# Optimization experiments

Hardware: AMD Instinct MI355X
Metric: run time of the kernel (lower is better)

## Reference

```python
import jax, jax.numpy as jnp
import numpy as np
import math

L = 16
DECAY = math.exp(-1.0 / 10.0)   # exp(-dt/tau)
THRESHOLD = 1.0
ALPHA = 0.01
EPS = 1e-6


def spike_fn(x):
    # MultiBitSurrogate forward: floor then clamp to [0, L]
    return jnp.clip(jnp.floor(x), 0.0, float(L))


def setup_inputs() -> dict:
    key = jax.random.key(0)
    k1, k2 = jax.random.split(key)
    B, S, D, H = 8, 4096, 512, 512
    x = jax.random.normal(k1, (B, S, D), dtype=jnp.float32)
    W = jax.random.normal(k2, (H, D), dtype=jnp.float32) * (1.0 / math.sqrt(D))
    b = jnp.zeros((H,), dtype=jnp.float32)
    return {"x": x, "W": W, "b": b}


def reference(x, W, b):
    B, S, D = x.shape
    H = W.shape[0]
    # dense input current for all timesteps: (B, S, H)
    h = jnp.einsum('bsd,hd->bsh', x, W) + b

    v0 = jnp.zeros((B, H), dtype=x.dtype)
    theta0 = jnp.full((B, H), THRESHOLD, dtype=x.dtype)

    def step(carry, i_t):
        v, theta = carry
        v = v * DECAY + i_t
        clamp_limit = L * theta * 2.0
        v = jnp.clip(v, -clamp_limit, clamp_limit)
        normalized_v = v / (theta + EPS)
        spike = spike_fn(normalized_v)
        v = v - spike * theta
        theta = theta + ALPHA * spike - ALPHA * (theta - THRESHOLD)
        return (v, theta), spike

    h_t = jnp.swapaxes(h, 0, 1)  # (S, B, H) for scan over time
    (v, theta), spikes = jax.lax.scan(step, (v0, theta0), h_t)
    spikes = jnp.swapaxes(spikes, 0, 1)  # (B, S, H)
    return spikes, v, theta
```

## Files before the change

kernel.cpp:

```cpp
#include <hip/hip_runtime.h>

#define B_DIM 8
#define S_LEN 4096
#define D_DIM 512
#define H_DIM 512

#define DECAY_F 0.90483743f
#define ALPHA_F 0.01f
#define EPS_F   1e-6f

#define KT 16
__global__ __launch_bounds__(256) void gemm_kernel(const float* __restrict__ x,
                                                   const float* __restrict__ W,
                                                   const float* __restrict__ bias,
                                                   float* __restrict__ out) {
    __shared__ float As[KT][132];
    __shared__ float Bs[KT][132];

    const int tid = threadIdx.x;
    const int waveId = tid >> 6;
    const int waveR = waveId & 1;
    const int waveC = waveId >> 1;
    const int lane = tid & 63;
    const int tr = lane >> 3;
    const int tc = lane & 7;
    const int rbase = waveR * 64 + tr * 8;
    const int c0 = waveC * 64 + tc * 4;
    const int c1 = c0 + 32;
    const int bm = blockIdx.y * 128;
    const int bn = blockIdx.x * 128;

    const int lrow = tid >> 2;
    const int lk4  = (tid & 3) * 4;

    const float* xa = &x[(size_t)(bm + lrow) * D_DIM + lk4];
    const float* xb = &x[(size_t)(bm + lrow + 64) * D_DIM + lk4];
    const float* wa = &W[(size_t)(bn + lrow) * D_DIM + lk4];
    const float* wb = &W[(size_t)(bn + lrow + 64) * D_DIM + lk4];

    float acc[8][8];
#pragma unroll
    for (int i = 0; i < 8; ++i)
#pragma unroll
        for (int j = 0; j < 8; ++j) acc[i][j] = 0.f;

    float4 a0 = *reinterpret_cast<const float4*>(xa);
    float4 a1 = *reinterpret_cast<const float4*>(xb);
    float4 b0 = *reinterpret_cast<const float4*>(wa);
    float4 b1 = *reinterpret_cast<const float4*>(wb);

    for (int kk = 0; kk < D_DIM; kk += KT) {
        __syncthreads();
        As[lk4 + 0][lrow]      = a0.x;
        As[lk4 + 1][lrow]      = a0.y;
        As[lk4 + 2][lrow]      = a0.z;
        As[lk4 + 3][lrow]      = a0.w;
        As[lk4 + 0][lrow + 64] = a1.x;
        As[lk4 + 1][lrow + 64] = a1.y;
        As[lk4 + 2][lrow + 64] = a1.z;
        As[lk4 + 3][lrow + 64] = a1.w;
        Bs[lk4 + 0][lrow]      = b0.x;
        Bs[lk4 + 1][lrow]      = b0.y;
        Bs[lk4 + 2][lrow]      = b0.z;
        Bs[lk4 + 3][lrow]      = b0.w;
        Bs[lk4 + 0][lrow + 64] = b1.x;
        Bs[lk4 + 1][lrow + 64] = b1.y;
        Bs[lk4 + 2][lrow + 64] = b1.z;
        Bs[lk4 + 3][lrow + 64] = b1.w;
        __syncthreads();

        if (kk + KT < D_DIM) {
            a0 = *reinterpret_cast<const float4*>(xa + kk + KT);
            a1 = *reinterpret_cast<const float4*>(xb + kk + KT);
            b0 = *reinterpret_cast<const float4*>(wa + kk + KT);
            b1 = *reinterpret_cast<const float4*>(wb + kk + KT);
        }

#pragma unroll
        for (int k = 0; k < KT; ++k) {
            const float4 av0 = *reinterpret_cast<const float4*>(&As[k][rbase]);
            const float4 av1 = *reinterpret_cast<const float4*>(&As[k][rbase + 4]);
            const float4 bv0 = *reinterpret_cast<const float4*>(&Bs[k][c0]);
            const float4 bv1 = *reinterpret_cast<const float4*>(&Bs[k][c1]);
            const float am[8]  = {av0.x, av0.y, av0.z, av0.w, av1.x, av1.y, av1.z, av1.w};
            const float bn_[8] = {bv0.x, bv0.y, bv0.z, bv0.w, bv1.x, bv1.y, bv1.z, bv1.w};
#pragma unroll
            for (int i = 0; i < 8; ++i)
#pragma unroll
                for (int j = 0; j < 8; ++j) acc[i][j] += am[i] * bn_[j];
        }
    }

    const float4 bias0 = *reinterpret_cast<const float4*>(&bias[bn + c0]);
    const float4 bias1 = *reinterpret_cast<const float4*>(&bias[bn + c1]);
    const float bb[8] = {bias0.x, bias0.y, bias0.z, bias0.w, bias1.x, bias1.y, bias1.z, bias1.w};

#pragma unroll
    for (int i = 0; i < 8; ++i) {
        const size_t row = (size_t)(bm + rbase + i);
        float4 o0, o1;
        o0.x = acc[i][0] + bb[0]; o0.y = acc[i][1] + bb[1];
        o0.z = acc[i][2] + bb[2]; o0.w = acc[i][3] + bb[3];
        o1.x = acc[i][4] + bb[4]; o1.y = acc[i][5] + bb[5];
        o1.z = acc[i][6] + bb[6]; o1.w = acc[i][7] + bb[7];
        *reinterpret_cast<float4*>(&out[row * H_DIM + bn + c0]) = o0;
        *reinterpret_cast<float4*>(&out[row * H_DIM + bn + c1]) = o1;
    }
}


__device__ __forceinline__ void stage_chunk(const float* __restrict__ gio, float* dstbase,
                                            int c, int lane) {
    const float* src = gio + (size_t)(c * 32 + (lane >> 4)) * H_DIM + ((lane & 15) << 2);
#pragma unroll
    for (int i = 0; i < 8; ++i) {
        __builtin_amdgcn_global_load_lds(
            (const __attribute__((address_space(1))) void*)(src + (size_t)i * 4 * H_DIM),
            (__attribute__((address_space(3))) void*)(dstbase + i * 256),
            16, 0, 0);
    }
}

__global__ __launch_bounds__(64, 1) void scan_kernel(float* __restrict__ io,
                                                     float* __restrict__ vout,
                                                     float* __restrict__ thout) {
    __shared__ float sbuf[2][32][64];

    const int lane = threadIdx.x;
    const int bi = blockIdx.x;
    const int b = bi >> 3;
    const int h0 = (bi & 7) << 6;

    float* gio = io + (size_t)b * S_LEN * H_DIM + h0;

    float v = 0.f;
    float theta = 1.f;
    float tden = theta + EPS_F;
    float rs = __builtin_amdgcn_rcpf(tden);
    float es = fmaf(-tden, rs, 1.0f);
    float r1 = fmaf(es, rs, rs);
    float es2 = fmaf(-tden, r1, 1.0f);
    float r0 = fmaf(es2, r1, r1);
    float cl = 32.f * theta;
    const float kSixteen = 16.0f;

    stage_chunk(gio, &sbuf[0][0][0], 0, lane);
    asm volatile("s_waitcnt vmcnt(0)" ::: "memory");

    const int NCHUNK = S_LEN / 32;
    for (int c = 0; c < NCHUNK; ++c) {
        if (c + 1 < NCHUNK) {
            stage_chunk(gio, &sbuf[(c + 1) & 1][0][0], c + 1, lane);
            asm volatile("s_waitcnt vmcnt(40)" ::: "memory");
        } else {
            asm volatile("s_waitcnt vmcnt(32)" ::: "memory");
        }
        __builtin_amdgcn_sched_barrier(0);

        const float* sb = &sbuf[c & 1][0][lane];
        float rr[32];
#pragma unroll
        for (int i = 0; i < 32; ++i) rr[i] = sb[i * 64];
        __builtin_amdgcn_sched_barrier(0);

        float* gout = gio + (size_t)c * 32 * H_DIM + lane;

#pragma unroll
        for (int u = 0; u < 32; ++u) {
            float vv = v * DECAY_F + rr[u];
            asm("v_med3_f32 %0, %0, -%1, %1" : "+v"(vv) : "v"(cl));
            v = vv;

            const float q0 = v * r0;
            const float e1 = fmaf(-tden, q0, v);
            const float nv = fmaf(e1, r0, q0);

            float spike = floorf(nv);
            asm("v_med3_f32 %0, %0, 0, %1" : "+v"(spike) : "v"(kSixteen));

            v = v - spike * theta;
            theta = theta + ALPHA_F * spike - ALPHA_F * (theta - 1.0f);

            tden = theta + EPS_F;
            const float rrcp = __builtin_amdgcn_rcpf(tden);
            const float ee = fmaf(-tden, rrcp, 1.0f);
            const float ra = fmaf(ee, rrcp, rrcp);
            const float ee2 = fmaf(-tden, ra, 1.0f);
            r0 = fmaf(ee2, ra, ra);
            cl = 32.f * theta;

            gout[(size_t)u * H_DIM] = spike;
        }
        __builtin_amdgcn_sched_barrier(0);
    }

    const int chain = b * H_DIM + h0 + lane;
    vout[chain]  = v;
    thout[chain] = theta;
}

extern "C" void kernel_launch(void* const* d_in, const int* in_sizes, int n_in,
                              void* d_out, int out_size, void* d_ws, size_t ws_size,
                              hipStream_t stream) {
    const float* x    = (const float*)d_in[0];
    const float* W    = (const float*)d_in[1];
    const float* bias = (const float*)d_in[2];

    float* out   = (float*)d_out;
    float* vout  = out + (size_t)B_DIM * S_LEN * H_DIM;
    float* thout = vout + B_DIM * H_DIM;

    dim3 grid(H_DIM / 128, (B_DIM * S_LEN) / 128);
    gemm_kernel<<<grid, 256, 0, stream>>>(x, W, bias, out);

    scan_kernel<<<64, 64, 0, stream>>>(out, vout, thout);
}
```

Before: 389.5 us.

## Fuse GEMM and scan into one persistent kernel with per-tile readiness flags

Merges the GEMM and the sequential scan into a single launch. Sixteen scan blocks, four waves each, spin on per-(batch, time-stripe) atomic flags and begin scanning as soon as GEMM blocks publish each 128-row stripe. This overlaps the latency-bound scan with GEMM work instead of running them back to back. The cost is a memset of the flags, spin-waiting blocks that hold CUs, and reliance on the scan blocks being scheduled early; it falls back to two launches when the workspace is too small.

```diff
diff --git a/kernel.cpp b/kernel.cpp
--- a/kernel.cpp
+++ b/kernel.cpp
@@ -10,13 +10,28 @@
 #define EPS_F   1e-6f
 
 #define KT 16
-__global__ __launch_bounds__(256) void gemm_kernel(const float* __restrict__ x,
-                                                   const float* __restrict__ W,
-                                                   const float* __restrict__ bias,
-                                                   float* __restrict__ out) {
-    __shared__ float As[KT][132];
-    __shared__ float Bs[KT][132];
-
+#define NCHUNK (S_LEN / 32)
+#define NSCAN_BLOCKS 16
+
+
+__device__ __forceinline__ void stage_chunk(const float* __restrict__ gio, float* dstbase,
+                                            int c, int lane) {
+    const float* src = gio + (size_t)(c * 32 + (lane >> 4)) * H_DIM + ((lane & 15) << 2);
+#pragma unroll
+    for (int i = 0; i < 8; ++i) {
+        __builtin_amdgcn_global_load_lds(
+            (const __attribute__((address_space(1))) void*)(src + (size_t)i * 4 * H_DIM),
+            (__attribute__((address_space(3))) void*)(dstbase + i * 256),
+            16, 0, 0);
+    }
+}
+
+__device__ __forceinline__ void gemm_tile(const float* __restrict__ x,
+                                          const float* __restrict__ W,
+                                          const float* __restrict__ bias,
+                                          float* __restrict__ out,
+                                          float (*As)[132], float (*Bs)[132],
+                                          int bm, int bn) {
     const int tid = threadIdx.x;
     const int waveId = tid >> 6;
     const int waveR = waveId & 1;
@@ -27,8 +42,6 @@
     const int rbase = waveR * 64 + tr * 8;
     const int c0 = waveC * 64 + tc * 4;
     const int c1 = c0 + 32;
-    const int bm = blockIdx.y * 128;
-    const int bn = blockIdx.x * 128;
 
     const int lrow = tid >> 2;
     const int lk4  = (tid & 3) * 4;
@@ -108,31 +121,10 @@
     }
 }
 
-
-__device__ __forceinline__ void stage_chunk(const float* __restrict__ gio, float* dstbase,
-                                            int c, int lane) {
-    const float* src = gio + (size_t)(c * 32 + (lane >> 4)) * H_DIM + ((lane & 15) << 2);
-#pragma unroll
-    for (int i = 0; i < 8; ++i) {
-        __builtin_amdgcn_global_load_lds(
-            (const __attribute__((address_space(1))) void*)(src + (size_t)i * 4 * H_DIM),
-            (__attribute__((address_space(3))) void*)(dstbase + i * 256),
-            16, 0, 0);
-    }
-}
-
-__global__ __launch_bounds__(64, 1) void scan_kernel(float* __restrict__ io,
-                                                     float* __restrict__ vout,
-                                                     float* __restrict__ thout) {
-    __shared__ float sbuf[2][32][64];
-
-    const int lane = threadIdx.x;
-    const int bi = blockIdx.x;
-    const int b = bi >> 3;
-    const int h0 = (bi & 7) << 6;
-
-    float* gio = io + (size_t)b * S_LEN * H_DIM + h0;
-
+__device__ __forceinline__ void scan_wave(float* __restrict__ gio, float* sbuf,
+                                          const int* flagrow, int lane,
+                                          float* __restrict__ vout,
+                                          float* __restrict__ thout, int chain) {
     float v = 0.f;
     float theta = 1.f;
     float tden = theta + EPS_F;
@@ -144,20 +136,32 @@
     float cl = 32.f * theta;
     const float kSixteen = 16.0f;
 
-    stage_chunk(gio, &sbuf[0][0][0], 0, lane);
+    if (flagrow) {
+        while (__hip_atomic_load(&flagrow[0], __ATOMIC_ACQUIRE, __HIP_MEMORY_SCOPE_AGENT) < 4)
+            __builtin_amdgcn_s_sleep(1);
+    }
+    stage_chunk(gio, sbuf, 0, lane);
     asm volatile("s_waitcnt vmcnt(0)" ::: "memory");
 
-    const int NCHUNK = S_LEN / 32;
     for (int c = 0; c < NCHUNK; ++c) {
         if (c + 1 < NCHUNK) {
-            stage_chunk(gio, &sbuf[(c + 1) & 1][0][0], c + 1, lane);
-            asm volatile("s_waitcnt vmcnt(40)" ::: "memory");
+            if (((c + 1) & 3) == 0 && flagrow) {
+                const int stn = (c + 1) >> 2;
+                while (__hip_atomic_load(&flagrow[stn], __ATOMIC_ACQUIRE,
+                                         __HIP_MEMORY_SCOPE_AGENT) < 4)
+                    __builtin_amdgcn_s_sleep(1);
+                asm volatile("s_waitcnt vmcnt(0)" ::: "memory");
+                stage_chunk(gio, sbuf + ((c + 1) & 1) * 2048, c + 1, lane);
+            } else {
+                stage_chunk(gio, sbuf + ((c + 1) & 1) * 2048, c + 1, lane);
+                asm volatile("s_waitcnt vmcnt(40)" ::: "memory");
+            }
         } else {
             asm volatile("s_waitcnt vmcnt(32)" ::: "memory");
         }
         __builtin_amdgcn_sched_barrier(0);
 
-        const float* sb = &sbuf[c & 1][0][lane];
+        const float* sb = sbuf + (c & 1) * 2048 + lane;
         float rr[32];
 #pragma unroll
         for (int i = 0; i < 32; ++i) rr[i] = sb[i * 64];
@@ -194,9 +198,78 @@
         __builtin_amdgcn_sched_barrier(0);
     }
 
-    const int chain = b * H_DIM + h0 + lane;
     vout[chain]  = v;
     thout[chain] = theta;
+}
+
+__global__ __launch_bounds__(256) void fused_kernel(const float* __restrict__ x,
+                                                    const float* __restrict__ W,
+                                                    const float* __restrict__ bias,
+                                                    float* __restrict__ out,
+                                                    float* __restrict__ vout,
+                                                    float* __restrict__ thout,
+                                                    int* __restrict__ flags) {
+    __shared__ __align__(16) char smem_raw[65536];
+    const int bid = blockIdx.x;
+
+    if (bid >= NSCAN_BLOCKS) {
+        float (*As)[132] = reinterpret_cast<float (*)[132]>(smem_raw);
+        float (*Bs)[132] = reinterpret_cast<float (*)[132]>(smem_raw + sizeof(float) * KT * 132);
+
+        const int g  = bid - NSCAN_BLOCKS;
+        const int st = g >> 5;
+        const int bb = (g >> 2) & 7;
+        const int nt = g & 3;
+        const int bm = bb * S_LEN + st * 128;
+        const int bn = nt * 128;
+
+        gemm_tile(x, W, bias, out, As, Bs, bm, bn);
+
+        __syncthreads();
+        if (threadIdx.x == 0) {
+            __hip_atomic_fetch_add(&flags[bb * 32 + st], 1,
+                                   __ATOMIC_RELEASE, __HIP_MEMORY_SCOPE_AGENT);
+        }
+        return;
+    }
+
+    const int w    = threadIdx.x >> 6;
+    const int lane = threadIdx.x & 63;
+    const int gi   = bid * 4 + w;
+    const int b    = gi >> 3;
+    const int h0   = (gi & 7) << 6;
+
+    float* sbuf = reinterpret_cast<float*>(smem_raw) + w * (2 * 32 * 64);
+    const int* flagrow = flags + b * 32;
+    float* gio = out + (size_t)b * S_LEN * H_DIM + h0;
+    const int chain = b * H_DIM + h0 + lane;
+
+    scan_wave(gio, sbuf, flagrow, lane, vout, thout, chain);
+}
+
+
+__global__ __launch_bounds__(256) void gemm_kernel(const float* __restrict__ x,
+                                                   const float* __restrict__ W,
+                                                   const float* __restrict__ bias,
+                                                   float* __restrict__ out) {
+    __shared__ float As[KT][132];
+    __shared__ float Bs[KT][132];
+    const int bm = blockIdx.y * 128;
+    const int bn = blockIdx.x * 128;
+    gemm_tile(x, W, bias, out, As, Bs, bm, bn);
+}
+
+__global__ __launch_bounds__(64, 1) void scan_kernel(float* __restrict__ io,
+                                                     float* __restrict__ vout,
+                                                     float* __restrict__ thout) {
+    __shared__ float sbuf[2][32][64];
+    const int lane = threadIdx.x;
+    const int bi = blockIdx.x;
+    const int b = bi >> 3;
+    const int h0 = (bi & 7) << 6;
+    float* gio = io + (size_t)b * S_LEN * H_DIM + h0;
+    const int chain = b * H_DIM + h0 + lane;
+    scan_wave(gio, &sbuf[0][0][0], nullptr, lane, vout, thout, chain);
 }
 
 extern "C" void kernel_launch(void* const* d_in, const int* in_sizes, int n_in,
@@ -210,8 +283,14 @@
     float* vout  = out + (size_t)B_DIM * S_LEN * H_DIM;
     float* thout = vout + B_DIM * H_DIM;
 
-    dim3 grid(H_DIM / 128, (B_DIM * S_LEN) / 128);
-    gemm_kernel<<<grid, 256, 0, stream>>>(x, W, bias, out);
-
-    scan_kernel<<<64, 64, 0, stream>>>(out, vout, thout);
-}
+    if (ws_size >= 1024) {
+        int* flags = (int*)d_ws;
+        hipMemsetAsync(flags, 0, 256 * sizeof(int), stream);
+        fused_kernel<<<NSCAN_BLOCKS + 1024, 256, 0, stream>>>(x, W, bias, out,
+                                                              vout, thout, flags);
+    } else {
+        dim3 grid(H_DIM / 128, (B_DIM * S_LEN) / 128);
+        gemm_kernel<<<grid, 256, 0, stream>>>(x, W, bias, out);
+        scan_kernel<<<64, 64, 0, stream>>>(out, vout, thout);
+    }
+}
```

Result: faster. 349.3 us (-10.3%).
